# Performance work log

Measured on AMD Instinct MI355X. Metric: run time of the kernel, lower is better.

## Reference

```python
import jax, jax.numpy as jnp
import numpy as np

SKIP = 91
PREEMPH = 0.85
N = 33554432  # 2**25 samples


def setup_inputs() -> dict:
    key = jax.random.key(0)
    sig = jax.random.normal(key, (N,), dtype=jnp.float32) * 0.1
    return {"sig": sig}


def _preemph_scan(y, coef):
    # First-order IIR: out[0] = y[0]; out[i] = y[i] + coef * out[i-1]
    # Expressed as an associative scan over pairs (a, b) representing x -> a*x + b.
    a = jnp.full_like(y, coef)

    def combine(e1, e2):
        a1, b1 = e1
        a2, b2 = e2
        return a1 * a2, b2 + a2 * b1

    _, out = jax.lax.associative_scan(combine, (a, y))
    return out


def reference(sig):
    y = _preemph_scan(sig, jnp.float32(PREEMPH))
    # drop first `skip` samples, zero-pad the tail (same length)
    y = jnp.concatenate([y[SKIP:], jnp.zeros((SKIP,), dtype=y.dtype)])
    out = jnp.clip(32768.0 * y, -32768.0, 32767.0).astype(jnp.int16)
    return out
```

## Files before the change

kernel.cpp:

```cpp
#include <hip/hip_runtime.h>


#define BLOCK   256
#define SKIP    91
#define COEF    0.85f
#define CHUNK_N 256
#define CHUNKS  8
#define SEG     (CHUNKS * CHUNK_N)
#define WPB     (BLOCK / 64)
#define TILE    (WPB * SEG)
#define NW      9
#define WFLOATS (NW * CHUNK_N)

typedef int v4i __attribute__((ext_vector_type(4)));
typedef __attribute__((address_space(3))) void       as3_void;
typedef const __attribute__((address_space(1))) void as1_void;

__device__ __forceinline__ int cvt16(float v) {
    float s = v * 32768.f;
    s = fminf(fmaxf(s, -32768.f), 32767.f);
    return (int)s;
}

__device__ __forceinline__ float chain4(const float4& v) {
    float a1 = fmaf(v.x, COEF, v.y);
    float a2 = fmaf(a1, COEF, v.z);
    return fmaf(a2, COEF, v.w);
}

template <int N>
__device__ __forceinline__ void wscan_multi(float (&t)[N], int lane) {
    const float K1  = COEF * COEF * COEF * COEF;
    const float K2  = K1 * K1, K4 = K2 * K2, K8 = K4 * K4, K16 = K8 * K8;
    const float KS[5] = {K1, K2, K4, K8, K16};
#pragma unroll
    for (int d = 0; d < 5; ++d) {
        const int sh = 1 << d;
        float u[N];
#pragma unroll
        for (int c = 0; c < N; ++c) u[c] = __shfl_up(t[c], sh, 64);
#pragma unroll
        for (int c = 0; c < N; ++c)
            t[c] = (lane >= sh) ? fmaf(u[c], KS[d], t[c]) : t[c];
    }
}

__device__ __forceinline__ float4 ld_guard(const float* __restrict__ sig,
                                           long yb, long n) {
    float4 x;
    x.x = (yb + 0 >= 0 && yb + 0 < n) ? sig[yb + 0] : 0.f;
    x.y = (yb + 1 >= 0 && yb + 1 < n) ? sig[yb + 1] : 0.f;
    x.z = (yb + 2 >= 0 && yb + 2 < n) ? sig[yb + 2] : 0.f;
    x.w = (yb + 3 >= 0 && yb + 3 < n) ? sig[yb + 3] : 0.f;
    return x;
}

__device__ void run_guard(const float* __restrict__ sig, int* __restrict__ out,
                          long segBase, long ln, int lane, float wq) {
    const float C1 = COEF, C2 = COEF * COEF, C3 = C2 * COEF;
    float4 x[9];
#pragma unroll
    for (int c = 0; c < 8; ++c)
        x[c] = ld_guard(sig, segBase + (SKIP + 1) + (long)c * CHUNK_N
                             + 4 * (long)lane, ln);
    x[8] = ld_guard(sig, segBase - 164 + 4 * (long)lane, ln);
    float t[9];
#pragma unroll
    for (int c = 0; c < 9; ++c) t[c] = chain4(x[c]);
    wscan_multi<9>(t, lane);
    float tsh[8], Tp[8];
#pragma unroll
    for (int c = 0; c < 8; ++c) tsh[c] = __shfl_up(t[c], 1, 64);
#pragma unroll
    for (int c = 0; c < 8; ++c) Tp[c] = __shfl(t[c == 0 ? 8 : c - 1], 63, 64);
    const long oLim = ln - SKIP;
#pragma unroll
    for (int c = 0; c < 8; ++c) {
        float u  = (lane == 0) ? 0.f : tsh[c];
        float p  = fmaf(Tp[c], wq, u);
        float s1 = fmaf(x[c].x, COEF, x[c].y);
        float s2 = fmaf(s1, COEF, x[c].z);
        v4i iv;
        iv.x = cvt16(p);
        iv.y = cvt16(fmaf(p, C1, x[c].x));
        iv.z = cvt16(fmaf(p, C2, s1));
        iv.w = cvt16(fmaf(p, C3, s2));
        const long ob = segBase + (long)c * CHUNK_N + 4 * (long)lane;
        if (ob + 0 >= oLim) iv.x = 0;
        if (ob + 1 >= oLim) iv.y = 0;
        if (ob + 2 >= oLim) iv.z = 0;
        if (ob + 3 >= oLim) iv.w = 0;
        if (ob + 0 < ln) out[ob + 0] = iv.x;
        if (ob + 1 < ln) out[ob + 1] = iv.y;
        if (ob + 2 < ln) out[ob + 2] = iv.z;
        if (ob + 3 < ln) out[ob + 3] = iv.w;
    }
}

__global__ __launch_bounds__(BLOCK, 4) void preemph_kernel(
        const float* __restrict__ sig, int* __restrict__ out, int n) {
    __shared__ float lds[WPB][WFLOATS];
    const long ln   = n;
    const int  lane = threadIdx.x & 63;
    const int  wid  = threadIdx.x >> 6;
    const long segBase = (long)blockIdx.x * TILE + (long)wid * SEG;
    if (segBase >= ln) return;

    const float wq = exp2f((float)lane * (4.0f * -0.23446525109f));

    const bool fast = (segBase >= 164) && (segBase + SEG + SKIP + 1 <= ln);
    if (!fast) { run_guard(sig, out, segBase, ln, lane, wq); return; }

    const float* gsrc = sig + (segBase - 164) + 4 * (long)lane;
    float* lb = &lds[wid][0];
#pragma unroll
    for (int w = 0; w < NW; ++w)
        __builtin_amdgcn_global_load_lds((as1_void*)(gsrc + w * CHUNK_N),
                                         (as3_void*)(lb + w * CHUNK_N),
                                         16, 0, 0);
    asm volatile("s_waitcnt vmcnt(0)" ::: "memory");
    __builtin_amdgcn_sched_barrier(0);

    float4 xw[NW];
    const float* lr = lb + 4 * lane;
#pragma unroll
    for (int w = 0; w < NW; ++w)
        xw[w] = *reinterpret_cast<const float4*>(lr + w * CHUNK_N);

    float t[NW];
#pragma unroll
    for (int w = 0; w < NW; ++w) t[w] = chain4(xw[w]);
    wscan_multi<NW>(t, lane);

    const float C1 = COEF, C2 = COEF * COEF, C3 = C2 * COEF;
#pragma unroll
    for (int c = 0; c < CHUNKS; ++c) {
        float tsh = __shfl_up(t[c + 1], 1, 64);
        float Tp  = __shfl(t[c], 63, 64);
        float u   = (lane == 0) ? 0.f : tsh;
        float p   = fmaf(Tp, wq, u);
        const float4 x = xw[c + 1];
        float s1 = fmaf(x.x, COEF, x.y);
        float s2 = fmaf(s1, COEF, x.z);
        v4i iv;
        iv.x = cvt16(p);
        iv.y = cvt16(fmaf(p, C1, x.x));
        iv.z = cvt16(fmaf(p, C2, s1));
        iv.w = cvt16(fmaf(p, C3, s2));
        *reinterpret_cast<v4i*>(out + segBase + c * CHUNK_N + 4 * (long)lane) = iv;
    }
}

extern "C" void kernel_launch(void* const* d_in, const int* in_sizes, int n_in,
                              void* d_out, int out_size, void* d_ws, size_t ws_size,
                              hipStream_t stream) {
    const float* sig = (const float*)d_in[0];
    int* out = (int*)d_out;
    int n = in_sizes[0];
    int grid = (int)(((long)n + TILE - 1) / TILE);
    preemph_kernel<<<grid, BLOCK, 0, stream>>>(sig, out, n);
}
```

Before: 231.8 us.

## Process consecutive tiles per wave with double-buffered LDS prefetch and carried scan state

Each wavefront now walks eight consecutive segments instead of one. The next segment's loads go into a second LDS buffer while the current one is computed. The scan carry (last prefix) is passed from one segment to the next, so only the first segment loads the 164-sample halo and later ones load just eight chunks. This cuts redundant halo reads and exposes load/compute overlap, at the cost of a smaller grid, a larger LDS footprint, lower occupancy (launch bounds 2) and hand-tuned vmcnt waits that depend on in-order counter accounting.

Result: slower. 238.8 us (+3.0%).

```diff
diff --git a/kernel.cpp b/kernel.cpp
--- a/kernel.cpp
+++ b/kernel.cpp
@@ -8,13 +8,15 @@
 #define CHUNKS  8
 #define SEG     (CHUNKS * CHUNK_N)
 #define WPB     (BLOCK / 64)
-#define TILE    (WPB * SEG)
+#define TPW     8
 #define NW      9
-#define WFLOATS (NW * CHUNK_N)
+#define BUF_F   (NW * CHUNK_N)
 
 typedef int v4i __attribute__((ext_vector_type(4)));
 typedef __attribute__((address_space(3))) void       as3_void;
 typedef const __attribute__((address_space(1))) void as1_void;
+
+#define VMWAIT(N) asm volatile("s_waitcnt vmcnt(" #N ")" ::: "memory")
 
 __device__ __forceinline__ int cvt16(float v) {
     float s = v * 32768.f;
@@ -43,6 +45,61 @@
         for (int c = 0; c < N; ++c)
             t[c] = (lane >= sh) ? fmaf(u[c], KS[d], t[c]) : t[c];
     }
+}
+
+__device__ __forceinline__ void emit_chunk(const float4& x, float tsh, float Tp,
+                                           int lane, float wq,
+                                           int* __restrict__ out, long ob) {
+    const float C1 = COEF, C2 = COEF * COEF, C3 = C2 * COEF;
+    float u = (lane == 0) ? 0.f : tsh;
+    float p = fmaf(Tp, wq, u);
+    float s1 = fmaf(x.x, COEF, x.y);
+    float s2 = fmaf(s1, COEF, x.z);
+    v4i iv;
+    iv.x = cvt16(p);
+    iv.y = cvt16(fmaf(p, C1, x.x));
+    iv.z = cvt16(fmaf(p, C2, s1));
+    iv.w = cvt16(fmaf(p, C3, s2));
+    *reinterpret_cast<v4i*>(out + ob) = iv;
+}
+
+__device__ __forceinline__ float compute9(const float* lb, int lane, float wq,
+                                          int* __restrict__ out, long segBase) {
+    const float* lr = lb + 4 * lane;
+    float4 xw[9];
+#pragma unroll
+    for (int w = 0; w < 9; ++w)
+        xw[w] = *reinterpret_cast<const float4*>(lr + w * CHUNK_N);
+    float t[9];
+#pragma unroll
+    for (int w = 0; w < 9; ++w) t[w] = chain4(xw[w]);
+    wscan_multi<9>(t, lane);
+#pragma unroll
+    for (int c = 0; c < 8; ++c)
+        emit_chunk(xw[c + 1], __shfl_up(t[c + 1], 1, 64), __shfl(t[c], 63, 64),
+                   lane, wq, out, segBase + c * CHUNK_N + 4 * (long)lane);
+    return t[8];
+}
+
+__device__ __forceinline__ float compute8(const float* lb, float tlast,
+                                          int lane, float wq,
+                                          int* __restrict__ out, long segBase) {
+    const float* lr = lb + 4 * lane;
+    float4 xw[8];
+#pragma unroll
+    for (int w = 0; w < 8; ++w)
+        xw[w] = *reinterpret_cast<const float4*>(lr + w * CHUNK_N);
+    float t[8];
+#pragma unroll
+    for (int w = 0; w < 8; ++w) t[w] = chain4(xw[w]);
+    wscan_multi<8>(t, lane);
+#pragma unroll
+    for (int c = 0; c < 8; ++c) {
+        float Tp = (c == 0) ? __shfl(tlast, 63, 64) : __shfl(t[c - 1], 63, 64);
+        emit_chunk(xw[c], __shfl_up(t[c], 1, 64), Tp,
+                   lane, wq, out, segBase + c * CHUNK_N + 4 * (long)lane);
+    }
+    return t[7];
 }
 
 __device__ __forceinline__ float4 ld_guard(const float* __restrict__ sig,
@@ -97,58 +154,62 @@
     }
 }
 
-__global__ __launch_bounds__(BLOCK, 4) void preemph_kernel(
+__device__ __forceinline__ bool fast_tile(long t, long ln) {
+    long sb = t * SEG;
+    return (sb >= 164) && (sb + SEG + SKIP + 1 <= ln);
+}
+
+__global__ __launch_bounds__(BLOCK, 2) void preemph_kernel(
         const float* __restrict__ sig, int* __restrict__ out, int n) {
-    __shared__ float lds[WPB][WFLOATS];
+    __shared__ float lds[WPB][2][BUF_F];
     const long ln   = n;
     const int  lane = threadIdx.x & 63;
     const int  wid  = threadIdx.x >> 6;
-    const long segBase = (long)blockIdx.x * TILE + (long)wid * SEG;
-    if (segBase >= ln) return;
+    const long ntiles = (ln + SEG - 1) / SEG;
+    const long t0 = ((long)blockIdx.x * WPB + wid) * TPW;
+    if (t0 >= ntiles) return;
+    const long t1 = (t0 + TPW < ntiles) ? t0 + TPW : ntiles;
 
     const float wq = exp2f((float)lane * (4.0f * -0.23446525109f));
 
-    const bool fast = (segBase >= 164) && (segBase + SEG + SKIP + 1 <= ln);
-    if (!fast) { run_guard(sig, out, segBase, ln, lane, wq); return; }
-
-    const float* gsrc = sig + (segBase - 164) + 4 * (long)lane;
-    float* lb = &lds[wid][0];
-#pragma unroll
-    for (int w = 0; w < NW; ++w)
-        __builtin_amdgcn_global_load_lds((as1_void*)(gsrc + w * CHUNK_N),
-                                         (as3_void*)(lb + w * CHUNK_N),
-                                         16, 0, 0);
-    asm volatile("s_waitcnt vmcnt(0)" ::: "memory");
-    __builtin_amdgcn_sched_barrier(0);
-
-    float4 xw[NW];
-    const float* lr = lb + 4 * lane;
-#pragma unroll
-    for (int w = 0; w < NW; ++w)
-        xw[w] = *reinterpret_cast<const float4*>(lr + w * CHUNK_N);
-
-    float t[NW];
-#pragma unroll
-    for (int w = 0; w < NW; ++w) t[w] = chain4(xw[w]);
-    wscan_multi<NW>(t, lane);
-
-    const float C1 = COEF, C2 = COEF * COEF, C3 = C2 * COEF;
-#pragma unroll
-    for (int c = 0; c < CHUNKS; ++c) {
-        float tsh = __shfl_up(t[c + 1], 1, 64);
-        float Tp  = __shfl(t[c], 63, 64);
-        float u   = (lane == 0) ? 0.f : tsh;
-        float p   = fmaf(Tp, wq, u);
-        const float4 x = xw[c + 1];
-        float s1 = fmaf(x.x, COEF, x.y);
-        float s2 = fmaf(s1, COEF, x.z);
-        v4i iv;
-        iv.x = cvt16(p);
-        iv.y = cvt16(fmaf(p, C1, x.x));
-        iv.z = cvt16(fmaf(p, C2, s1));
-        iv.w = cvt16(fmaf(p, C3, s2));
-        *reinterpret_cast<v4i*>(out + segBase + c * CHUNK_N + 4 * (long)lane) = iv;
-    }
+    long cl = t0, cr = t1;
+    while (cl < cr && !fast_tile(cl, ln)) { run_guard(sig, out, cl * SEG, ln, lane, wq); ++cl; }
+    while (cr > cl && !fast_tile(cr - 1, ln)) --cr;
+
+    if (cl < cr) {
+        float* b0 = &lds[wid][0][0];
+        float* b1 = &lds[wid][1][0];
+
+        const float* g9 = sig + cl * SEG - 164 + 4 * (long)lane;
+#pragma unroll
+        for (int w = 0; w < 9; ++w)
+            __builtin_amdgcn_global_load_lds((as1_void*)(g9 + w * CHUNK_N),
+                                             (as3_void*)(b0 + w * CHUNK_N),
+                                             16, 0, 0);
+        float tlast = 0.f;
+        int par = 0;
+        for (long t = cl; t < cr; ++t) {
+            const bool first = (t == cl), hasN = (t + 1 < cr);
+            if (hasN) {
+                const float* g8 = sig + (t + 1) * SEG + (SKIP + 1) + 4 * (long)lane;
+                float* nb = par ? b0 : b1;
+#pragma unroll
+                for (int c = 0; c < 8; ++c)
+                    __builtin_amdgcn_global_load_lds((as1_void*)(g8 + c * CHUNK_N),
+                                                     (as3_void*)(nb + c * CHUNK_N),
+                                                     16, 0, 0);
+            }
+            if (first) { if (hasN) VMWAIT(8);  else VMWAIT(0); }
+            else       { if (hasN) VMWAIT(16); else VMWAIT(8); }
+            __builtin_amdgcn_sched_barrier(0);
+
+            const float* cb = par ? b1 : b0;
+            if (first) tlast = compute9(cb, lane, wq, out, t * SEG);
+            else       tlast = compute8(cb, tlast, lane, wq, out, t * SEG);
+            par ^= 1;
+        }
+    }
+    for (long t = cr; t < t1; ++t) run_guard(sig, out, t * SEG, ln, lane, wq);
 }
 
 extern "C" void kernel_launch(void* const* d_in, const int* in_sizes, int n_in,
@@ -157,6 +218,7 @@
     const float* sig = (const float*)d_in[0];
     int* out = (int*)d_out;
     int n = in_sizes[0];
-    int grid = (int)(((long)n + TILE - 1) / TILE);
+    long ntiles = ((long)n + SEG - 1) / SEG;
+    int grid = (int)((ntiles + (long)WPB * TPW - 1) / ((long)WPB * TPW));
     preemph_kernel<<<grid, BLOCK, 0, stream>>>(sig, out, n);
 }
```
